# Kernel optimization log

Hardware: AMD Instinct MI355X
Metric: run time of the kernel (lower is better)

Reference implementation:

```python
import jax, jax.numpy as jnp
import numpy as np

B, T, F, H, L = 512, 512, 64, 128, 3


def setup_inputs() -> dict:
    key = jax.random.key(0)
    ks = jax.random.split(key, 6)
    s_in = 1.0 / np.sqrt(F)
    s_h = 1.0 / np.sqrt(H)
    return {
        "x": jax.random.normal(ks[0], (B, T, F), dtype=jnp.float32),
        "Wx0": jax.random.normal(ks[1], (F, 3 * H), dtype=jnp.float32) * s_in,
        "Wx_rest": jax.random.normal(ks[2], (L - 1, H, 3 * H), dtype=jnp.float32) * s_h,
        "Wh": jax.random.normal(ks[3], (L, H, 3 * H), dtype=jnp.float32) * s_h,
        "b": jnp.zeros((L, 3 * H), dtype=jnp.float32),
        "Wd": jax.random.normal(ks[4], (H, H), dtype=jnp.float32) * s_h,
        "bd": jnp.zeros((H,), dtype=jnp.float32),
    }


def _gru_layer(x_seq, Wx, Wh_l, b_l):
    """x_seq: [T, B, Din] -> [T, B, H]. Classic GRU (reset_after=False)."""
    # Precompute input projections for all timesteps in one GEMM: [T, B, 3H]
    gx = jnp.einsum("tbd,dg->tbg", x_seq, Wx) + b_l

    def step(h, gx_t):
        gh = h @ Wh_l                      # [B, 3H]
        xz, xr, xn = jnp.split(gx_t, 3, axis=-1)
        hz, hr, hn = jnp.split(gh, 3, axis=-1)
        z = jax.nn.sigmoid(xz + hz)
        r = jax.nn.sigmoid(xr + hr)
        n = jnp.tanh(xn + r * hn)
        h_new = z * h + (1.0 - z) * n
        return h_new, h_new

    h0 = jnp.zeros((x_seq.shape[1], Wh_l.shape[0]), dtype=x_seq.dtype)
    _, hs = jax.lax.scan(step, h0, gx)
    return hs                              # [T, B, H]


def reference(x, Wx0, Wx_rest, Wh, b, Wd, bd):
    h = jnp.swapaxes(x, 0, 1)              # [T, B, F] time-major for scan
    h = _gru_layer(h, Wx0, Wh[0], b[0])
    for l in range(1, L):                  # small fixed layer loop
        h = _gru_layer(h, Wx_rest[l - 1], Wh[l], b[l])
    h = jnp.swapaxes(h, 0, 1)              # [B, T, H]
    return jax.nn.sigmoid(jnp.einsum("bth,hk->btk", h, Wd) + bd)
```

## Files before the change

kernel.cpp:

```cpp
#include <hip/hip_runtime.h>

namespace {

constexpr int Bb = 512, Tt = 512, Ff = 64, Hh = 128, Gg = 384;
constexpr int CH = 64, NCH = Tt / CH;
constexpr float SZ = -1.44269504f;
constexpr float SN =  2.88539008f;

using short8  = __attribute__((ext_vector_type(8))) short;
using short4v = __attribute__((ext_vector_type(4))) short;
using f32x4   = __attribute__((ext_vector_type(4))) float;

__device__ __forceinline__ short f2bf(float f) {
  unsigned u = __float_as_uint(f);
  u += 0x7FFFu + ((u >> 16) & 1u);
  return (short)(u >> 16);
}
__device__ __forceinline__ float bf2f(short s) {
  return __uint_as_float(((unsigned)(unsigned short)s) << 16);
}

__global__ __launch_bounds__(512, 4) void prep(const float* __restrict__ Wx0,
                                               const float* __restrict__ Wxr,
                                               const float* __restrict__ Wh,
                                               const float* __restrict__ Wd,
                                               char* __restrict__ WhF,
                                               char* __restrict__ WxF,
                                               char* __restrict__ WdF) {
  const int id = blockIdx.x * 512 + threadIdx.x;
  const int lane = id & 63, lr = lane & 15, lk = lane >> 4;
  const int q = id >> 6;
  const float* src; int col, ldn, row0; char* dst; float sc;
  if (q < 288) {
    const int l = q / 96, rem = q % 96, w = rem / 12, f = rem % 12;
    const int g = f >> 2, ks = f & 3;
    src = Wh + (size_t)l * Hh * Gg; ldn = Gg;
    col = g * 128 + w * 16 + lr; row0 = ks * 32 + lk * 8;
    dst = WhF + (size_t)(q * 64 + lane) * 16;
    sc = (g < 2) ? SZ : SN;
  } else if (q < 528) {
    int p = q - 288; int base;
    if (p < 48)       { src = Wx0; base = 0; }
    else if (p < 144) { src = Wxr; base = 48; p -= 48; }
    else              { src = Wxr + (size_t)Hh * Gg; base = 144; p -= 144; }
    int ct, ks;
    if (base == 0) { ct = p >> 1; ks = p & 1; } else { ct = p >> 2; ks = p & 3; }
    ldn = Gg; col = ct * 16 + lr; row0 = ks * 32 + lk * 8;
    dst = WxF + (size_t)((base + p) * 64 + lane) * 16;
    sc = (ct < 16) ? SZ : SN;
  } else {
    const int p = q - 528;
    const int ct = p >> 2, ks = p & 3;
    src = Wd; ldn = Hh; col = ct * 16 + lr; row0 = ks * 32 + lk * 8;
    dst = WdF + (size_t)(p * 64 + lane) * 16;
    sc = SZ;
  }
  short8 v;
#pragma unroll
  for (int j = 0; j < 8; ++j) v[j] = f2bf(src[(size_t)(row0 + j) * ldn + col] * sc);
  *(short8*)dst = v;
}

template <int KS>
__device__ void gemm_phase(const void* __restrict__ src, int t0,
                           const char* __restrict__ wxf,
                           const float* __restrict__ bias,
                           char* __restrict__ gx,
                           int rb, int w, int lane, int lr, int lk) {
  short8 bw[3][KS];
  float bs[3];
#pragma unroll
  for (int c = 0; c < 3; ++c) {
    const int ct = w * 3 + c;
    bs[c] = bias[ct * 16 + lr] * (ct < 16 ? SZ : SN);
#pragma unroll
    for (int ks = 0; ks < KS; ++ks)
      bw[c][ks] = *(const short8*)(wxf + (size_t)((ct * KS + ks) * 64 + lane) * 16);
  }
#pragma unroll 2
  for (int t = 0; t < CH; ++t) {
    short8 af[KS];
    if constexpr (KS == 2) {
      const float* xr = (const float*)src;
#pragma unroll
      for (int ks = 0; ks < 2; ++ks) {
        const float* p = xr + ((size_t)(rb * 16 + lr) * Tt + t0 + t) * Ff + ks * 32 + lk * 8;
        f32x4 u0 = *(const f32x4*)p, u1 = *(const f32x4*)(p + 4);
        short8 v;
#pragma unroll
        for (int j = 0; j < 4; ++j) { v[j] = f2bf(u0[j]); v[4 + j] = f2bf(u1[j]); }
        af[ks] = v;
      }
    } else {
      const char* hr = (const char*)src;
#pragma unroll
      for (int ks = 0; ks < 4; ++ks)
        af[ks] = *(const short8*)(hr + ((size_t)t * 512 + rb * 16 + lr) * 256 +
                                  ((ks * 64 + lk * 16) ^ ((lr & 7) << 4)));
    }
#pragma unroll
    for (int c = 0; c < 3; ++c) {
      f32x4 acc = {0.f, 0.f, 0.f, 0.f};
#pragma unroll
      for (int ks = 0; ks < KS; ++ks)
        acc = __builtin_amdgcn_mfma_f32_16x16x32_bf16(af[ks], bw[c][ks], acc, 0, 0, 0);
      const int ct = w * 3 + c;
      short4v o;
#pragma unroll
      for (int i = 0; i < 4; ++i) o[i] = f2bf(acc[i] + bs[c]);
      *(short4v*)(gx + (size_t)((t * 32 + rb) * 8 + (ct & 7)) * 1536 + lane * 24 + (ct >> 3) * 8) = o;
    }
  }
}

__device__ void scan_phase(const char* __restrict__ gx,
                           const char* __restrict__ whf,
                           short* __restrict__ hstream,
                           float* __restrict__ state, int t0, int dense,
                           const char* __restrict__ wdf,
                           const float* __restrict__ bdp,
                           float* __restrict__ out,
                           int rb, char* hb, int* cnt) {
  const int tid = threadIdx.x;
  const int w = tid >> 6, lane = tid & 63, lr = lane & 15, lk = lane >> 4;
  const int col = w * 16 + lr;

  short8 bwh[3][4];
#pragma unroll
  for (int g = 0; g < 3; ++g)
#pragma unroll
    for (int ks = 0; ks < 4; ++ks)
      bwh[g][ks] = *(const short8*)(whf + (size_t)((w * 12 + g * 4 + ks) * 64 + lane) * 16);

  short8 bwd[4]; float bdv = 0.f;
  if (dense) {
#pragma unroll
    for (int ks = 0; ks < 4; ++ks)
      bwd[ks] = *(const short8*)(wdf + (size_t)((w * 4 + ks) * 64 + lane) * 16);
    bdv = bdp[col] * SZ;
  }

  int hoffs[4];
#pragma unroll
  for (int i = 0; i < 4; ++i) {
    const int row = lk * 4 + i;
    hoffs[i] = row * 256 + ((col * 2) ^ ((row & 7) << 4));
  }

  if (tid == 0) *cnt = 0;

  float hreg[4];
  if (t0 == 0) {
#pragma unroll
    for (int i = 0; i < 4; ++i) hreg[i] = 0.f;
    short* hz = (short*)hb;
    for (int i = tid; i < 2048; i += 512) hz[i] = 0;
  } else {
    f32x4 s = *(const f32x4*)(state + (size_t)(rb * 512 + tid) * 4);
#pragma unroll
    for (int i = 0; i < 4; ++i) {
      hreg[i] = s[i];
      *(short*)(hb + hoffs[i]) = f2bf(s[i]);
    }
  }

  const char* gp = gx + (size_t)(rb * 8 + w) * 1536 + lane * 24;
  short4v pf0[3], pf1[3], pf2[3], pf3[3];
#pragma unroll
  for (int j = 0; j < 3; ++j) pf0[j] = *(const short4v*)(gp + j * 8);
#pragma unroll
  for (int j = 0; j < 3; ++j) pf1[j] = *(const short4v*)(gp + 393216 + j * 8);
  __syncthreads();

  auto WAIT = [&](int target) {
    int budget = 1 << 22;
    while (__hip_atomic_load(cnt, __ATOMIC_RELAXED, __HIP_MEMORY_SCOPE_WORKGROUP) < target &&
           --budget) {}
    __builtin_amdgcn_sched_barrier(0);
  };

  auto STEP = [&](int s, short4v (&use)[3], short4v (&fill)[3]) {
    const int pin = s & 1;
    const char* hsrc = hb + pin * 4096;
    char* const hdst = hb + (1 - pin) * 4096;
    const int tg = t0 + s;

    if (s > 0) {
      WAIT(8 * s);
      if (!dense) {
        short4v hv = *(const short4v*)(hsrc + tid * 8);
        *(short4v*)(hstream + ((size_t)(s - 1) * 512 + rb * 16 + (tid >> 5)) * 128 +
                    (tid & 31) * 4) = hv;
      }
    }

    short8 ah[4];
#pragma unroll
    for (int ks = 0; ks < 4; ++ks)
      ah[ks] = *(const short8*)(hsrc + lr * 256 + ((ks * 64 + lk * 16) ^ ((lr & 7) << 4)));

    f32x4 aZ = {0.f, 0.f, 0.f, 0.f}, aR = aZ, aHn = aZ;
#pragma unroll
    for (int ks = 0; ks < 4; ++ks) {
      aZ  = __builtin_amdgcn_mfma_f32_16x16x32_bf16(ah[ks], bwh[0][ks], aZ, 0, 0, 0);
      aR  = __builtin_amdgcn_mfma_f32_16x16x32_bf16(ah[ks], bwh[1][ks], aR, 0, 0, 0);
      aHn = __builtin_amdgcn_mfma_f32_16x16x32_bf16(ah[ks], bwh[2][ks], aHn, 0, 0, 0);
    }
    if (s + 2 < CH) {
      const char* p = gp + (size_t)(s + 2) * 393216;
      fill[0] = *(const short4v*)p;
      fill[1] = *(const short4v*)(p + 8);
      fill[2] = *(const short4v*)(p + 16);
    }
    if (dense && tg > 0) {
      f32x4 aD = {0.f, 0.f, 0.f, 0.f};
#pragma unroll
      for (int ks = 0; ks < 4; ++ks)
        aD = __builtin_amdgcn_mfma_f32_16x16x32_bf16(ah[ks], bwd[ks], aD, 0, 0, 0);
#pragma unroll
      for (int i = 0; i < 4; ++i)
        out[((size_t)(rb * 16 + lk * 4 + i) * Tt + (tg - 1)) * Hh + col] =
            __builtin_amdgcn_rcpf(1.f + __builtin_amdgcn_exp2f(aD[i] + bdv));
    }

    float hn4[4];
#pragma unroll
    for (int i = 0; i < 4; ++i) {
      const float z  = __builtin_amdgcn_rcpf(1.f + __builtin_amdgcn_exp2f(aZ[i] + bf2f(use[0][i])));
      const float rr = __builtin_amdgcn_rcpf(1.f + __builtin_amdgcn_exp2f(aR[i] + bf2f(use[1][i])));
      const float eu = __builtin_amdgcn_exp2f(__builtin_fmaf(rr, aHn[i], bf2f(use[2][i])));
      const float nn = __builtin_fmaf(-2.f, __builtin_amdgcn_rcpf(1.f + eu), 1.f);
      const float h  = __builtin_fmaf(z, hreg[i] - nn, nn);
      hn4[i] = h; hreg[i] = h;
    }
    unsigned p01, p23;
    asm("v_cvt_pk_bf16_f32 %0, %1, %2" : "=v"(p01) : "v"(hn4[0]), "v"(hn4[1]));
    asm("v_cvt_pk_bf16_f32 %0, %1, %2" : "=v"(p23) : "v"(hn4[2]), "v"(hn4[3]));
    *(short*)(hdst + hoffs[0]) = (short)(p01 & 0xffffu);
    *(short*)(hdst + hoffs[1]) = (short)(p01 >> 16);
    *(short*)(hdst + hoffs[2]) = (short)(p23 & 0xffffu);
    *(short*)(hdst + hoffs[3]) = (short)(p23 >> 16);

    __builtin_amdgcn_sched_barrier(0);
    asm volatile("s_waitcnt lgkmcnt(0)");
    __builtin_amdgcn_sched_barrier(0);
    if (lane == 0) atomicAdd(cnt, 1);
    __builtin_amdgcn_sched_barrier(0);
  };

  for (int tb = 0; tb < CH; tb += 4) {
    STEP(tb + 0, pf0, pf2);
    STEP(tb + 1, pf1, pf3);
    STEP(tb + 2, pf2, pf0);
    STEP(tb + 3, pf3, pf1);
  }

  WAIT(8 * CH);

  {
    f32x4 sv;
#pragma unroll
    for (int i = 0; i < 4; ++i) sv[i] = hreg[i];
    *(f32x4*)(state + (size_t)(rb * 512 + tid) * 4) = sv;
  }
  if (!dense) {
    short4v hv = *(const short4v*)(hb + tid * 8);
    *(short4v*)(hstream + ((size_t)(CH - 1) * 512 + rb * 16 + (tid >> 5)) * 128 +
                (tid & 31) * 4) = hv;
  } else if (t0 + CH == Tt) {
    short8 ah[4];
#pragma unroll
    for (int ks = 0; ks < 4; ++ks)
      ah[ks] = *(const short8*)(hb + lr * 256 + ((ks * 64 + lk * 16) ^ ((lr & 7) << 4)));
    f32x4 aD = {0.f, 0.f, 0.f, 0.f};
#pragma unroll
    for (int ks = 0; ks < 4; ++ks)
      aD = __builtin_amdgcn_mfma_f32_16x16x32_bf16(ah[ks], bwd[ks], aD, 0, 0, 0);
#pragma unroll
    for (int i = 0; i < 4; ++i)
      out[((size_t)(rb * 16 + lk * 4 + i) * Tt + (Tt - 1)) * Hh + col] =
          __builtin_amdgcn_rcpf(1.f + __builtin_amdgcn_exp2f(aD[i] + bdv));
  }
}

struct LArgs {
  const void* src; const char* wxf; const char* whf; const float* bias;
  char* gx; short* hstream; float* state; int t0; int ksx; int dense;
};

__global__ __launch_bounds__(512, 1) void fused(LArgs a0, LArgs a1, LArgs a2,
                                                const char* __restrict__ wdf,
                                                const float* __restrict__ bd,
                                                float* __restrict__ out) {
  __shared__ char hb[8192];
  __shared__ int  cnt;
  const int g = blockIdx.x >> 5;
  const int rb = blockIdx.x & 31;
  LArgs a = (g == 0) ? a0 : (g == 1 ? a1 : a2);
  const int tid = threadIdx.x;
  const int w = tid >> 6, lane = tid & 63, lr = lane & 15, lk = lane >> 4;

  if (a.ksx == 2) gemm_phase<2>(a.src, a.t0, a.wxf, a.bias, a.gx, rb, w, lane, lr, lk);
  else            gemm_phase<4>(a.src, a.t0, a.wxf, a.bias, a.gx, rb, w, lane, lr, lk);

  __builtin_amdgcn_sched_barrier(0);
  asm volatile("s_waitcnt vmcnt(0)");
  __builtin_amdgcn_s_barrier();
  __builtin_amdgcn_sched_barrier(0);

  scan_phase(a.gx, a.whf, a.hstream, a.state, a.t0, a.dense, wdf, bd, out,
             rb, hb, &cnt);
}

}

extern "C" void kernel_launch(void* const* d_in, const int* in_sizes, int n_in,
                              void* d_out, int out_size, void* d_ws, size_t ws_size,
                              hipStream_t stream) {
  const float* x   = (const float*)d_in[0];
  const float* Wx0 = (const float*)d_in[1];
  const float* Wxr = (const float*)d_in[2];
  const float* Wh  = (const float*)d_in[3];
  const float* b   = (const float*)d_in[4];
  const float* Wd  = (const float*)d_in[5];
  const float* bd  = (const float*)d_in[6];
  float* out = (float*)d_out;

  char* ws = (char*)d_ws;
  char*  WhF    = ws;
  char*  WxF    = ws + 294912;
  char*  WdF    = ws + 540672;
  float* state0 = (float*)(ws + 573440);
  char*  gx0    = ws + 1441792;
  char*  gx1    = gx0 + 25165824;
  char*  gx2    = gx1 + 25165824;
  short* hc     = (short*)(ws + 76939264);

  prep<<<70, 512, 0, stream>>>(Wx0, Wxr, Wh, Wd, WhF, WxF, WdF);

  const size_t WXOFF[3] = {0, 49152, 147456};
  for (int r = 0; r < NCH + 2; ++r) {
    LArgs la[3]; int n = 0;
    for (int l = 0; l < 3; ++l) {
      const int k = r - l;
      if (k < 0 || k >= NCH) continue;
      LArgs& A = la[n++];
      A.src = (l == 0) ? (const void*)x
                       : (const void*)(hc + (size_t)((l - 1) * 2 + (k & 1)) * 4194304);
      A.wxf = WxF + WXOFF[l];
      A.whf = WhF + (size_t)l * 98304;
      A.bias = b + l * Gg;
      A.gx = (l == 0) ? gx0 : (l == 1 ? gx1 : gx2);
      A.hstream = (l < 2) ? hc + (size_t)(l * 2 + (k & 1)) * 4194304 : nullptr;
      A.state = state0 + l * 65536;
      A.t0 = k * CH;
      A.ksx = (l == 0) ? 2 : 4;
      A.dense = (l == 2) ? 1 : 0;
    }
    for (int i = n; i < 3; ++i) la[i] = la[0];
    fused<<<n * 32, 512, 0, stream>>>(la[0], la[1], la[2], WdF, bd, out);
  }
}
```

Before: 1.259 ms.

## Pack two independent scan teams into one 1024-thread workgroup

Each workgroup now holds two 512-thread teams, each handling its own row block with its own LDS hidden-state buffer and step counter, which halves the grid size. The aim is to put two latency-bound recurrent scans on one CU so one team's MFMA and memory latency can overlap the other's. The risk is that register pressure at 1024 threads forces spills of the preloaded weight fragments, and the shared s_barrier after the gemm phase now couples the two teams.

```diff
diff --git a/kernel.cpp b/kernel.cpp
--- a/kernel.cpp
+++ b/kernel.cpp
@@ -120,9 +120,8 @@
                            const char* __restrict__ wdf,
                            const float* __restrict__ bdp,
                            float* __restrict__ out,
-                           int rb, char* hb, int* cnt) {
-  const int tid = threadIdx.x;
-  const int w = tid >> 6, lane = tid & 63, lr = lane & 15, lk = lane >> 4;
+                           int rb, int ltid, char* hb, int* cnt) {
+  const int w = ltid >> 6, lane = ltid & 63, lr = lane & 15, lk = lane >> 4;
   const int col = w * 16 + lr;
 
   short8 bwh[3][4];
@@ -147,16 +146,16 @@
     hoffs[i] = row * 256 + ((col * 2) ^ ((row & 7) << 4));
   }
 
-  if (tid == 0) *cnt = 0;
+  if (ltid == 0) *cnt = 0;
 
   float hreg[4];
   if (t0 == 0) {
 #pragma unroll
     for (int i = 0; i < 4; ++i) hreg[i] = 0.f;
     short* hz = (short*)hb;
-    for (int i = tid; i < 2048; i += 512) hz[i] = 0;
+    for (int i = ltid; i < 2048; i += 512) hz[i] = 0;
   } else {
-    f32x4 s = *(const f32x4*)(state + (size_t)(rb * 512 + tid) * 4);
+    f32x4 s = *(const f32x4*)(state + (size_t)(rb * 512 + ltid) * 4);
 #pragma unroll
     for (int i = 0; i < 4; ++i) {
       hreg[i] = s[i];
@@ -188,9 +187,9 @@
     if (s > 0) {
       WAIT(8 * s);
       if (!dense) {
-        short4v hv = *(const short4v*)(hsrc + tid * 8);
-        *(short4v*)(hstream + ((size_t)(s - 1) * 512 + rb * 16 + (tid >> 5)) * 128 +
-                    (tid & 31) * 4) = hv;
+        short4v hv = *(const short4v*)(hsrc + ltid * 8);
+        *(short4v*)(hstream + ((size_t)(s - 1) * 512 + rb * 16 + (ltid >> 5)) * 128 +
+                    (ltid & 31) * 4) = hv;
       }
     }
 
@@ -261,12 +260,12 @@
     f32x4 sv;
 #pragma unroll
     for (int i = 0; i < 4; ++i) sv[i] = hreg[i];
-    *(f32x4*)(state + (size_t)(rb * 512 + tid) * 4) = sv;
+    *(f32x4*)(state + (size_t)(rb * 512 + ltid) * 4) = sv;
   }
   if (!dense) {
-    short4v hv = *(const short4v*)(hb + tid * 8);
-    *(short4v*)(hstream + ((size_t)(CH - 1) * 512 + rb * 16 + (tid >> 5)) * 128 +
-                (tid & 31) * 4) = hv;
+    short4v hv = *(const short4v*)(hb + ltid * 8);
+    *(short4v*)(hstream + ((size_t)(CH - 1) * 512 + rb * 16 + (ltid >> 5)) * 128 +
+                (ltid & 31) * 4) = hv;
   } else if (t0 + CH == Tt) {
     short8 ah[4];
 #pragma unroll
@@ -288,17 +287,19 @@
   char* gx; short* hstream; float* state; int t0; int ksx; int dense;
 };
 
-__global__ __launch_bounds__(512, 1) void fused(LArgs a0, LArgs a1, LArgs a2,
-                                                const char* __restrict__ wdf,
-                                                const float* __restrict__ bd,
-                                                float* __restrict__ out) {
-  __shared__ char hb[8192];
-  __shared__ int  cnt;
-  const int g = blockIdx.x >> 5;
-  const int rb = blockIdx.x & 31;
+__global__ __launch_bounds__(1024, 1) void fused(LArgs a0, LArgs a1, LArgs a2,
+                                                 const char* __restrict__ wdf,
+                                                 const float* __restrict__ bd,
+                                                 float* __restrict__ out) {
+  __shared__ char hb[2][8192];
+  __shared__ int  cnt[2][16];
+  const int g = blockIdx.x >> 4;
   LArgs a = (g == 0) ? a0 : (g == 1 ? a1 : a2);
   const int tid = threadIdx.x;
-  const int w = tid >> 6, lane = tid & 63, lr = lane & 15, lk = lane >> 4;
+  const int team = tid >> 9;
+  const int ltid = tid & 511;
+  const int rb = (blockIdx.x & 15) * 2 + team;
+  const int w = ltid >> 6, lane = ltid & 63, lr = lane & 15, lk = lane >> 4;
 
   if (a.ksx == 2) gemm_phase<2>(a.src, a.t0, a.wxf, a.bias, a.gx, rb, w, lane, lr, lk);
   else            gemm_phase<4>(a.src, a.t0, a.wxf, a.bias, a.gx, rb, w, lane, lr, lk);
@@ -309,7 +310,7 @@
   __builtin_amdgcn_sched_barrier(0);
 
   scan_phase(a.gx, a.whf, a.hstream, a.state, a.t0, a.dense, wdf, bd, out,
-             rb, hb, &cnt);
+             rb, ltid, hb[team], &cnt[team][0]);
 }
 
 }
@@ -358,6 +359,6 @@
       A.dense = (l == 2) ? 1 : 0;
     }
     for (int i = n; i < 3; ++i) la[i] = la[0];
-    fused<<<n * 32, 512, 0, stream>>>(la[0], la[1], la[2], WdF, bd, out);
-  }
-}
+    fused<<<n * 16, 1024, 0, stream>>>(la[0], la[1], la[2], WdF, bd, out);
+  }
+}
```

Result: slower. 2.680 ms (+112.9%).
